# Kernel optimization log

Measured on AMD Instinct MI355X. Metric: run time of the kernel, lower is better.

Reference implementation:

```python
import jax, jax.numpy as jnp
from jax import lax
import numpy as np

EPS = 1e-5

def lc2d(x, w, b, stride):
    # x: [B,H,W]; w: [oh,ow,kh,kw] unshared kernels; b: [oh,ow]
    oh, ow, kh, kw = w.shape
    hi = jnp.arange(oh)[:, None] * stride + jnp.arange(kh)[None, :]  # [oh,kh]
    wi = jnp.arange(ow)[:, None] * stride + jnp.arange(kw)[None, :]  # [ow,kw]
    patches = x[:, hi[:, None, :, None], wi[None, :, None, :]]  # [B,oh,ow,kh,kw]
    return jnp.einsum('bhwkl,hwkl->bhw', patches, w) + b

def ln2d(x, g, b):
    # LayerNorm over last two dims (per-sample)
    m = jnp.mean(x, axis=(-2, -1), keepdims=True)
    v = jnp.var(x, axis=(-2, -1), keepdims=True)
    return (x - m) * lax.rsqrt(v + EPS) * g + b

def maxpool2(x):
    # MaxPool2d(kernel=2, stride=2) on [B,H,W]
    return lax.reduce_window(x, -jnp.inf, lax.max, (1, 2, 2), (1, 2, 2), 'VALID')

def setup_inputs() -> dict:
    key = jax.random.key(0)
    ks = iter(jax.random.split(key, 16))
    d = {'x': jax.random.normal(next(ks), (128, 224, 224), jnp.float32)}
    layer_specs = [(109, 7), (50, 5), (48, 3), (22, 3), (20, 3), (8, 3)]
    for i, (o, k) in enumerate(layer_specs, 1):
        std = float(np.sqrt(2.0 / (k + k)))  # xavier_normal_ on a [k,k] kernel
        d[f'w{i}'] = jax.random.normal(next(ks), (o, o, k, k), jnp.float32) * std
        d[f'b{i}'] = jnp.zeros((o, o), jnp.float32)
        d[f'g{i}'] = jnp.ones((o, o), jnp.float32)
        d[f'be{i}'] = jnp.zeros((o, o), jnp.float32)
    d['fcw'] = jax.random.normal(next(ks), (1000, 64), jnp.float32) * float(np.sqrt(1.0 / 64))
    d['fcb'] = jnp.zeros((1000,), jnp.float32)
    return d

def reference(x, w1, b1, g1, be1, w2, b2, g2, be2, w3, b3, g3, be3,
              w4, b4, g4, be4, w5, b5, g5, be5, w6, b6, g6, be6, fcw, fcb):
    # dropout is inference-mode identity (p=0)
    h = ln2d(jax.nn.relu(lc2d(x, w1, b1, 2)), g1, be1)   # [B,109,109]
    h = maxpool2(h)                                       # [B,54,54]
    h = ln2d(jax.nn.relu(lc2d(h, w2, b2, 1)), g2, be2)   # [B,50,50]
    h = ln2d(jax.nn.relu(lc2d(h, w3, b3, 1)), g3, be3)   # [B,48,48]
    h = maxpool2(h)                                       # [B,24,24]
    h = ln2d(jax.nn.relu(lc2d(h, w4, b4, 1)), g4, be4)   # [B,22,22]
    h = ln2d(jax.nn.relu(lc2d(h, w5, b5, 1)), g5, be5)   # [B,20,20]
    h = maxpool2(h)                                       # [B,10,10]
    h = ln2d(jax.nn.relu(lc2d(h, w6, b6, 1)), g6, be6)   # [B,8,8]
    logits = h.reshape(h.shape[0], -1) @ fcw.T + fcb      # [B,1000]
    return jax.nn.softmax(logits, axis=1)
```

## Files before the change

### kernel.cpp

```cpp
#include <hip/hip_runtime.h>
#include <math.h>

static constexpr float kEps = 1e-5f;

__global__ __launch_bounds__(256)
void xpose(const float* __restrict__ x, float* __restrict__ xt,
           const float* __restrict__ w2, const float* __restrict__ w3,
           const float* __restrict__ w4, const float* __restrict__ w5,
           const float* __restrict__ w6,
           const float* __restrict__ g1, const float* __restrict__ be1,
           float* __restrict__ w2t, float* __restrict__ w3t,
           float* __restrict__ w4t, float* __restrict__ w5t,
           float* __restrict__ w6t,
           float4* __restrict__ g1p, float4* __restrict__ be1p)
{
    const int bid = blockIdx.x, t = threadIdx.x;
    if (bid >= 784) {
        const int tid = (bid - 784) * 256 + t;
        const int nt  = 14 * 256;
        for (int i = tid; i < 25 * 50 * 52; i += nt) {
            const int kk = i / (50 * 52), r = i % (50 * 52);
            const int oh = r / 52, ow = r % 52;
            w2t[i] = (ow < 50) ? w2[(oh * 50 + ow) * 25 + kk] : 0.f;
        }
        for (int i = tid; i < 9 * 2304; i += nt) {
            const int kk = i / 2304, idx = i % 2304;
            w3t[i] = w3[idx * 9 + kk];
        }
        for (int i = tid; i < 9 * 22 * 24; i += nt) {
            const int kk = i / (22 * 24), r = i % (22 * 24);
            const int oh = r / 24, ow = r % 24;
            w4t[i] = (ow < 22) ? w4[(oh * 22 + ow) * 9 + kk] : 0.f;
        }
        for (int i = tid; i < 9 * 400; i += nt) {
            const int kk = i / 400, idx = i % 400;
            w5t[i] = w5[idx * 9 + kk];
        }
        for (int i = tid; i < 9 * 64; i += nt) {
            const int kk = i / 64, idx = i % 64;
            w6t[i] = w6[idx * 9 + kk];
        }
        for (int i = tid; i < 54 * 54; i += nt) {
            const int ph = i / 54, pw = i - ph * 54;
            const int i00 = (2 * ph) * 109 + 2 * pw, i10 = i00 + 109;
            g1p[i]  = make_float4(g1[i00],  g1[i00 + 1],  g1[i10],  g1[i10 + 1]);
            be1p[i] = make_float4(be1[i00], be1[i00 + 1], be1[i10], be1[i10 + 1]);
        }
        return;
    }

    __shared__ float ls[64 * 133];
    const int pos0 = bid * 64;
    for (int i = t; i < 8192; i += 256) {
        const int s = i >> 6, j = i & 63;
        ls[j * 133 + s] = x[(size_t)s * 50176 + pos0 + j];
    }
    __syncthreads();
    for (int i = t; i < 8192; i += 256) {
        const int j = i >> 7, s = i & 127;
        xt[(size_t)(pos0 + j) * 128 + s] = ls[j * 133 + s];
    }
}

__global__ __launch_bounds__(512)
void conv1(const float* __restrict__ xt, const float* __restrict__ w1,
           const float* __restrict__ bias, float* __restrict__ y,
           float* __restrict__ partial)
{
    __shared__ float redS[8][64], redQ[8][64];
    const int oh = blockIdx.x;
    const int grp = blockIdx.y;
    const int t = threadIdx.x;
    const int w = t >> 6, lane = t & 63;
    const int smp = grp * 64 + lane;

    float lsum = 0.f, lsq = 0.f;
    for (int ch = w; ch < 28; ch += 8) {
        const int ow0 = ch * 4;
        float xv[7][13];
        const size_t base = ((size_t)(2 * oh) * 224 + 2 * ow0) * 128 + smp;
        #pragma unroll
        for (int r = 0; r < 7; ++r) {
            #pragma unroll
            for (int c = 0; c < 13; ++c)
                xv[r][c] = xt[base + ((size_t)(r * 224 + c)) * 128];
        }
        #pragma unroll
        for (int o = 0; o < 4; ++o) {
            const int ow = ow0 + o;
            if (ow < 109) {
                const int idx = __builtin_amdgcn_readfirstlane(oh * 109 + ow);
                const float* __restrict__ wr = w1 + (size_t)idx * 49;
                float acc = bias[idx];
                #pragma unroll
                for (int kh = 0; kh < 7; ++kh) {
                    #pragma unroll
                    for (int kw = 0; kw < 7; ++kw)
                        acc = fmaf(xv[kh][2 * o + kw], wr[kh * 7 + kw], acc);
                }
                const float v = fmaxf(acc, 0.f);
                y[((size_t)smp * 109 + oh) * 112 + ow] = v;
                lsum += v; lsq = fmaf(v, v, lsq);
            }
        }
    }
    redS[w][lane] = lsum; redQ[w][lane] = lsq;
    __syncthreads();
    if (w == 0) {
        float s = 0.f, q = 0.f;
        #pragma unroll
        for (int i = 0; i < 8; ++i) { s += redS[i][lane]; q += redQ[i][lane]; }
        *(float2*)(partial + ((size_t)smp * 109 + oh) * 2) = make_float2(s, q);
    }
}

__device__ inline float2 bstats(float ls, float lq, float invN, float (*red)[2], int t)
{
    #pragma unroll
    for (int off = 32; off > 0; off >>= 1) {
        ls += __shfl_down(ls, off, 64);
        lq += __shfl_down(lq, off, 64);
    }
    if ((t & 63) == 0) { red[t >> 6][0] = ls; red[t >> 6][1] = lq; }
    __syncthreads();
    float s = 0.f, q = 0.f;
    #pragma unroll
    for (int w = 0; w < 16; ++w) { s += red[w][0]; q += red[w][1]; }
    const float m = s * invN;
    return make_float2(m, rsqrtf(q * invN - m * m + kEps));
}

__global__ __launch_bounds__(1024)
void tail(const float* __restrict__ y1, const float* __restrict__ partial,
          const float4* __restrict__ g1p, const float4* __restrict__ be1p,
          const float* __restrict__ w2t, const float* __restrict__ b2,
          const float* __restrict__ g2, const float* __restrict__ be2,
          const float* __restrict__ w3t, const float* __restrict__ b3,
          const float* __restrict__ g3, const float* __restrict__ be3,
          const float* __restrict__ w4t, const float* __restrict__ b4,
          const float* __restrict__ g4, const float* __restrict__ be4,
          const float* __restrict__ w5t, const float* __restrict__ b5,
          const float* __restrict__ g5, const float* __restrict__ be5,
          const float* __restrict__ w6t, const float* __restrict__ b6,
          const float* __restrict__ g6, const float* __restrict__ be6,
          const float* __restrict__ fcw, const float* __restrict__ fcb,
          float* __restrict__ out)
{
    __shared__ __align__(16) float xs54[54 * 54 + 8];
    __shared__ __align__(16) float y50[50 * 52];
    __shared__ __align__(16) float y48[48 * 48];
    __shared__ __align__(16) float xs24[24 * 24 + 8];
    __shared__ __align__(16) float y22[22 * 24];
    __shared__ __align__(16) float y20[20 * 20];
    __shared__ __align__(16) float xs10[100];
    __shared__ float y8[64], h[64];
    __shared__ float red[16][2];

    const int b = blockIdx.x, t = threadIdx.x;
    const int lane = t & 63;

    float s, q;
    {
        const float2 p = *(const float2*)(partial + ((size_t)b * 109 + lane) * 2);
        s = p.x; q = p.y;
        if (lane < 45) {
            const float2 p2 = *(const float2*)(partial + ((size_t)b * 109 + 64 + lane) * 2);
            s += p2.x; q += p2.y;
        }
    }
    #pragma unroll
    for (int off = 32; off > 0; off >>= 1) {
        s += __shfl_down(s, off, 64);
        q += __shfl_down(q, off, 64);
    }
    s = __shfl(s, 0, 64); q = __shfl(q, 0, 64);
    const float m1 = s / 11881.f;
    const float r1 = rsqrtf(q / 11881.f - m1 * m1 + kEps);

    const float* yb = y1 + (size_t)b * 109 * 112;
    #pragma unroll
    for (int it = 0; it < 3; ++it) {
        const int idx = t + it * 1024;
        if (idx < 54 * 54) {
            const int ph = idx / 54, pw = idx - ph * 54;
            const int r0 = 2 * ph, c0 = 2 * pw;
            const float2 u0 = *(const float2*)(yb + r0 * 112 + c0);
            const float2 u1 = *(const float2*)(yb + (r0 + 1) * 112 + c0);
            const float4 g = g1p[idx], be = be1p[idx];
            const float v0 = (u0.x - m1) * r1 * g.x + be.x;
            const float v1 = (u0.y - m1) * r1 * g.y + be.y;
            const float v2 = (u1.x - m1) * r1 * g.z + be.z;
            const float v3 = (u1.y - m1) * r1 * g.w + be.w;
            xs54[ph * 54 + pw] = fmaxf(fmaxf(v0, v1), fmaxf(v2, v3));
        }
    }
    __syncthreads();

    float ls = 0.f, lq = 0.f;
    if (t < 650) {
        const int oh = t / 13, qc = t - oh * 13;
        const int ow0 = qc * 4;
        float acc[4];
        #pragma unroll
        for (int o = 0; o < 4; ++o) acc[o] = (ow0 + o < 50) ? b2[oh * 50 + ow0 + o] : 0.f;
        #pragma unroll
        for (int kh = 0; kh < 5; ++kh) {
            const float* xp = xs54 + (oh + kh) * 54 + ow0;
            float a[8];
            #pragma unroll
            for (int i = 0; i < 4; ++i) {
                const float2 v = *(const float2*)(xp + 2 * i);
                a[2 * i] = v.x; a[2 * i + 1] = v.y;
            }
            #pragma unroll
            for (int kw = 0; kw < 5; ++kw) {
                const float4 w4 = *(const float4*)(w2t + ((size_t)(kh * 5 + kw) * 50 + oh) * 52 + ow0);
                acc[0] = fmaf(a[kw    ], w4.x, acc[0]);
                acc[1] = fmaf(a[kw + 1], w4.y, acc[1]);
                acc[2] = fmaf(a[kw + 2], w4.z, acc[2]);
                acc[3] = fmaf(a[kw + 3], w4.w, acc[3]);
            }
        }
        #pragma unroll
        for (int o = 0; o < 4; ++o) {
            const float v = fmaxf(acc[o], 0.f);
            y50[oh * 52 + ow0 + o] = v;
            if (ow0 + o < 50) { ls += v; lq = fmaf(v, v, lq); }
        }
    }
    const float2 s2 = bstats(ls, lq, 1.f / 2500.f, red, t);

    #pragma unroll
    for (int it = 0; it < 3; ++it) {
        const int idx = t + it * 1024;
        if (idx < 2500) {
            const int oh = idx / 50, ow = idx - oh * 50;
            const int p = oh * 52 + ow;
            y50[p] = (y50[p] - s2.x) * s2.y * g2[idx] + be2[idx];
        }
    }
    __syncthreads();

    ls = 0.f; lq = 0.f;
    if (t < 576) {
        const int oh = t / 12, qc = t - oh * 12;
        const int ow0 = qc * 4;
        float acc[4];
        #pragma unroll
        for (int o = 0; o < 4; ++o) acc[o] = b3[oh * 48 + ow0 + o];
        #pragma unroll
        for (int kh = 0; kh < 3; ++kh) {
            const float* xp = y50 + (oh + kh) * 52 + ow0;
            float a[6];
            #pragma unroll
            for (int i = 0; i < 3; ++i) {
                const float2 v = *(const float2*)(xp + 2 * i);
                a[2 * i] = v.x; a[2 * i + 1] = v.y;
            }
            #pragma unroll
            for (int kw = 0; kw < 3; ++kw) {
                const float4 w4 = *(const float4*)(w3t + (size_t)(kh * 3 + kw) * 2304 + oh * 48 + ow0);
                acc[0] = fmaf(a[kw    ], w4.x, acc[0]);
                acc[1] = fmaf(a[kw + 1], w4.y, acc[1]);
                acc[2] = fmaf(a[kw + 2], w4.z, acc[2]);
                acc[3] = fmaf(a[kw + 3], w4.w, acc[3]);
            }
        }
        float4 st;
        #pragma unroll
        for (int o = 0; o < 4; ++o) {
            const float v = fmaxf(acc[o], 0.f);
            (&st.x)[o] = v; ls += v; lq = fmaf(v, v, lq);
        }
        *(float4*)(y48 + oh * 48 + ow0) = st;
    }
    const float2 s3 = bstats(ls, lq, 1.f / 2304.f, red, t);

    if (t < 576) {
        const int ph = t / 24, pw = t - ph * 24;
        const int r0 = 2 * ph, c0 = 2 * pw;
        const float2 u0 = *(const float2*)(y48 + r0 * 48 + c0);
        const float2 u1 = *(const float2*)(y48 + (r0 + 1) * 48 + c0);
        const int i00 = r0 * 48 + c0, i10 = i00 + 48;
        const float v0 = (u0.x - s3.x) * s3.y * g3[i00]     + be3[i00];
        const float v1 = (u0.y - s3.x) * s3.y * g3[i00 + 1] + be3[i00 + 1];
        const float v2 = (u1.x - s3.x) * s3.y * g3[i10]     + be3[i10];
        const float v3 = (u1.y - s3.x) * s3.y * g3[i10 + 1] + be3[i10 + 1];
        xs24[ph * 24 + pw] = fmaxf(fmaxf(v0, v1), fmaxf(v2, v3));
    }
    __syncthreads();

    ls = 0.f; lq = 0.f;
    if (t < 132) {
        const int oh = t / 6, qc = t - oh * 6;
        const int ow0 = qc * 4;
        float acc[4];
        #pragma unroll
        for (int o = 0; o < 4; ++o) acc[o] = (ow0 + o < 22) ? b4[oh * 22 + ow0 + o] : 0.f;
        #pragma unroll
        for (int kh = 0; kh < 3; ++kh) {
            const float* xp = xs24 + (oh + kh) * 24 + ow0;
            float a[6];
            #pragma unroll
            for (int i = 0; i < 3; ++i) {
                const float2 v = *(const float2*)(xp + 2 * i);
                a[2 * i] = v.x; a[2 * i + 1] = v.y;
            }
            #pragma unroll
            for (int kw = 0; kw < 3; ++kw) {
                const float4 w4 = *(const float4*)(w4t + ((size_t)(kh * 3 + kw) * 22 + oh) * 24 + ow0);
                acc[0] = fmaf(a[kw    ], w4.x, acc[0]);
                acc[1] = fmaf(a[kw + 1], w4.y, acc[1]);
                acc[2] = fmaf(a[kw + 2], w4.z, acc[2]);
                acc[3] = fmaf(a[kw + 3], w4.w, acc[3]);
            }
        }
        #pragma unroll
        for (int o = 0; o < 4; ++o) {
            const float v = fmaxf(acc[o], 0.f);
            y22[oh * 24 + ow0 + o] = v;
            if (ow0 + o < 22) { ls += v; lq = fmaf(v, v, lq); }
        }
    }
    const float2 s4 = bstats(ls, lq, 1.f / 484.f, red, t);

    if (t < 484) {
        const int oh = t / 22, ow = t - oh * 22;
        const int p = oh * 24 + ow;
        y22[p] = (y22[p] - s4.x) * s4.y * g4[t] + be4[t];
    }
    __syncthreads();

    ls = 0.f; lq = 0.f;
    if (t < 100) {
        const int oh = t / 5, qc = t - oh * 5;
        const int ow0 = qc * 4;
        float acc[4];
        #pragma unroll
        for (int o = 0; o < 4; ++o) acc[o] = b5[oh * 20 + ow0 + o];
        #pragma unroll
        for (int kh = 0; kh < 3; ++kh) {
            const float* xp = y22 + (oh + kh) * 24 + ow0;
            float a[6];
            #pragma unroll
            for (int i = 0; i < 3; ++i) {
                const float2 v = *(const float2*)(xp + 2 * i);
                a[2 * i] = v.x; a[2 * i + 1] = v.y;
            }
            #pragma unroll
            for (int kw = 0; kw < 3; ++kw) {
                const float4 w4 = *(const float4*)(w5t + (size_t)(kh * 3 + kw) * 400 + oh * 20 + ow0);
                acc[0] = fmaf(a[kw    ], w4.x, acc[0]);
                acc[1] = fmaf(a[kw + 1], w4.y, acc[1]);
                acc[2] = fmaf(a[kw + 2], w4.z, acc[2]);
                acc[3] = fmaf(a[kw + 3], w4.w, acc[3]);
            }
        }
        #pragma unroll
        for (int o = 0; o < 4; ++o) {
            const float v = fmaxf(acc[o], 0.f);
            y20[oh * 20 + ow0 + o] = v;
            ls += v; lq = fmaf(v, v, lq);
        }
    }
    const float2 s5 = bstats(ls, lq, 1.f / 400.f, red, t);

    if (t < 100) {
        const int ph = t / 10, pw = t - ph * 10;
        const int r0 = 2 * ph, c0 = 2 * pw;
        const float2 u0 = *(const float2*)(y20 + r0 * 20 + c0);
        const float2 u1 = *(const float2*)(y20 + (r0 + 1) * 20 + c0);
        const int i00 = r0 * 20 + c0, i10 = i00 + 20;
        const float v0 = (u0.x - s5.x) * s5.y * g5[i00]     + be5[i00];
        const float v1 = (u0.y - s5.x) * s5.y * g5[i00 + 1] + be5[i00 + 1];
        const float v2 = (u1.x - s5.x) * s5.y * g5[i10]     + be5[i10];
        const float v3 = (u1.y - s5.x) * s5.y * g5[i10 + 1] + be5[i10 + 1];
        xs10[ph * 10 + pw] = fmaxf(fmaxf(v0, v1), fmaxf(v2, v3));
    }
    __syncthreads();

    ls = 0.f; lq = 0.f;
    if (t < 16) {
        const int oh = t / 2, qc = t - oh * 2;
        const int ow0 = qc * 4;
        float acc[4];
        #pragma unroll
        for (int o = 0; o < 4; ++o) acc[o] = b6[oh * 8 + ow0 + o];
        #pragma unroll
        for (int kh = 0; kh < 3; ++kh) {
            const float* xp = xs10 + (oh + kh) * 10 + ow0;
            float a[6];
            #pragma unroll
            for (int i = 0; i < 3; ++i) {
                const float2 v = *(const float2*)(xp + 2 * i);
                a[2 * i] = v.x; a[2 * i + 1] = v.y;
            }
            #pragma unroll
            for (int kw = 0; kw < 3; ++kw) {
                const float4 w4 = *(const float4*)(w6t + (size_t)(kh * 3 + kw) * 64 + oh * 8 + ow0);
                acc[0] = fmaf(a[kw    ], w4.x, acc[0]);
                acc[1] = fmaf(a[kw + 1], w4.y, acc[1]);
                acc[2] = fmaf(a[kw + 2], w4.z, acc[2]);
                acc[3] = fmaf(a[kw + 3], w4.w, acc[3]);
            }
        }
        #pragma unroll
        for (int o = 0; o < 4; ++o) {
            const float v = fmaxf(acc[o], 0.f);
            y8[oh * 8 + ow0 + o] = v;
            ls += v; lq = fmaf(v, v, lq);
        }
    }
    const float2 s6 = bstats(ls, lq, 1.f / 64.f, red, t);

    if (t < 64) h[t] = (y8[t] - s6.x) * s6.y * g6[t] + be6[t];
    __syncthreads();

    float lj = -INFINITY;
    if (t < 1000) {
        const float4* wr = (const float4*)(fcw + (size_t)t * 64);
        float acc = fcb[t];
        #pragma unroll
        for (int k = 0; k < 16; ++k) {
            const float4 w4 = wr[k];
            acc = fmaf(h[4 * k], w4.x,
                  fmaf(h[4 * k + 1], w4.y,
                  fmaf(h[4 * k + 2], w4.z,
                  fmaf(h[4 * k + 3], w4.w, acc))));
        }
        lj = acc;
    }
    float mx = lj;
    #pragma unroll
    for (int off = 32; off > 0; off >>= 1) mx = fmaxf(mx, __shfl_down(mx, off, 64));
    if (lane == 0) red[t >> 6][0] = mx;
    __syncthreads();
    float gmax = red[0][0];
    #pragma unroll
    for (int w = 1; w < 16; ++w) gmax = fmaxf(gmax, red[w][0]);

    const float e = (t < 1000) ? __expf(lj - gmax) : 0.f;
    float ssum = e;
    #pragma unroll
    for (int off = 32; off > 0; off >>= 1) ssum += __shfl_down(ssum, off, 64);
    if (lane == 0) red[t >> 6][1] = ssum;
    __syncthreads();
    float tot = 0.f;
    #pragma unroll
    for (int w = 0; w < 16; ++w) tot += red[w][1];
    if (t < 1000) out[(size_t)b * 1000 + t] = e / tot;
}

extern "C" void kernel_launch(void* const* d_in, const int* in_sizes, int n_in,
                              void* d_out, int out_size, void* d_ws, size_t ws_size,
                              hipStream_t stream) {
    const float* x   = (const float*)d_in[0];
    const float* w1  = (const float*)d_in[1];
    const float* b1  = (const float*)d_in[2];
    const float* g1  = (const float*)d_in[3];
    const float* be1 = (const float*)d_in[4];
    const float* w2  = (const float*)d_in[5];
    const float* b2  = (const float*)d_in[6];
    const float* g2  = (const float*)d_in[7];
    const float* be2 = (const float*)d_in[8];
    const float* w3  = (const float*)d_in[9];
    const float* b3  = (const float*)d_in[10];
    const float* g3  = (const float*)d_in[11];
    const float* be3 = (const float*)d_in[12];
    const float* w4  = (const float*)d_in[13];
    const float* b4  = (const float*)d_in[14];
    const float* g4  = (const float*)d_in[15];
    const float* be4 = (const float*)d_in[16];
    const float* w5  = (const float*)d_in[17];
    const float* b5  = (const float*)d_in[18];
    const float* g5  = (const float*)d_in[19];
    const float* be5 = (const float*)d_in[20];
    const float* w6  = (const float*)d_in[21];
    const float* b6  = (const float*)d_in[22];
    const float* g6  = (const float*)d_in[23];
    const float* be6 = (const float*)d_in[24];
    const float* fcw = (const float*)d_in[25];
    const float* fcb = (const float*)d_in[26];

    float* xt   = (float*)d_ws;
    float* y1p  = xt   + 6422528;
    float* w2t  = y1p  + 1562624;
    float* w3t  = w2t  + 65000;
    float* w4t  = w3t  + 20736;
    float* w5t  = w4t  + 4752;
    float* w6t  = w5t  + 3600;
    float* part = w6t  + 576;
    float* g1pp = part + 27904;
    float* be1pp= g1pp + 11664;

    xpose<<<798, 256, 0, stream>>>(x, xt,
                                   w2, w3, w4, w5, w6, g1, be1,
                                   w2t, w3t, w4t, w5t, w6t,
                                   (float4*)g1pp, (float4*)be1pp);

    conv1<<<dim3(109, 2), 512, 0, stream>>>(xt, w1, b1, y1p, part);

    tail<<<128, 1024, 0, stream>>>(y1p, part,
                                   (const float4*)g1pp, (const float4*)be1pp,
                                   w2t, b2, g2, be2,
                                   w3t, b3, g3, be3,
                                   w4t, b4, g4, be4,
                                   w5t, b5, g5, be5,
                                   w6t, b6, g6, be6,
                                   fcw, fcb, (float*)d_out);
}
```

Before: 64.65 us.

## Retile conv1 into 2D output tiles with shared-memory input staging

conv1 now launches a 3D grid of 16x37x2 blocks. Each block covers a 3-row by 7-column output tile for 64 samples, and it stages the overlapping input window into shared memory as float2 pairs before computing. Before, each thread loaded 91 values per 4 outputs straight from global memory, so this cuts redundant global reads and spreads work over more blocks (1184 instead of 218) to use the GPU better. The per-row partial stats become per-tile partials (592 per sample), and the tail kernel now reduces them with a block-wide bstats call. In exchange this adds more partial traffic, uses about 56KB of LDS per block, and leaves some threads idle on edge tiles.

```diff
diff --git a/kernel.cpp b/kernel.cpp
--- a/kernel.cpp
+++ b/kernel.cpp
@@ -62,55 +62,95 @@
     }
 }
 
-__global__ __launch_bounds__(512)
+__global__ __launch_bounds__(384)
 void conv1(const float* __restrict__ xt, const float* __restrict__ w1,
            const float* __restrict__ bias, float* __restrict__ y,
            float* __restrict__ partial)
 {
-    __shared__ float redS[8][64], redQ[8][64];
-    const int oh = blockIdx.x;
-    const int grp = blockIdx.y;
+    constexpr int NPB = 592;
+    __shared__ float2 xin2[11 * 10 * 64];
+    __shared__ float redS[6][64], redQ[6][64];
+
+    const int ct = blockIdx.x;
+    const int rg = blockIdx.y;
+    const int sg = blockIdx.z;
     const int t = threadIdx.x;
-    const int w = t >> 6, lane = t & 63;
-    const int smp = grp * 64 + lane;
+    const int w = t >> 6, s = t & 63;
+    const int smp0 = sg * 64;
+    const int ow0 = ct * 7;
+    const int or0 = rg * 3;
+    const int ih0 = or0 * 2;
+    const int ic0 = ow0 * 2;
+
+    for (int i = t; i < 7040; i += 384) {
+        const int seg = i >> 6, ls = i & 63;
+        const int r = seg / 10, cp = seg - r * 10;
+        const int row = min(ih0 + r, 223);
+        const int c0 = ic0 + 2 * cp;
+        const int ca = min(c0, 223), cb = min(c0 + 1, 223);
+        const float vx = xt[((size_t)row * 224 + ca) * 128 + smp0 + ls];
+        const float vy = xt[((size_t)row * 224 + cb) * 128 + smp0 + ls];
+        xin2[seg * 64 + ls] = make_float2(vx, vy);
+    }
+    __syncthreads();
 
     float lsum = 0.f, lsq = 0.f;
-    for (int ch = w; ch < 28; ch += 8) {
-        const int ow0 = ch * 4;
-        float xv[7][13];
-        const size_t base = ((size_t)(2 * oh) * 224 + 2 * ow0) * 128 + smp;
-        #pragma unroll
-        for (int r = 0; r < 7; ++r) {
-            #pragma unroll
-            for (int c = 0; c < 13; ++c)
-                xv[r][c] = xt[base + ((size_t)(r * 224 + c)) * 128];
-        }
-        #pragma unroll
-        for (int o = 0; o < 4; ++o) {
-            const int ow = ow0 + o;
-            if (ow < 109) {
-                const int idx = __builtin_amdgcn_readfirstlane(oh * 109 + ow);
-                const float* __restrict__ wr = w1 + (size_t)idx * 49;
-                float acc = bias[idx];
+    {
+        const int r = w >> 1, half = w & 1;
+        const int orow = or0 + r;
+        const int oc0 = half ? 3 : 0;
+        const int noc = half ? 4 : 3;
+        const int pr0 = half ? 3 : 0;
+        const int npr = half ? 7 : 6;
+        if (orow < 109) {
+            float acc[4];
+            int idxo[4];
+            #pragma unroll
+            for (int oc = 0; oc < 4; ++oc) {
+                const int ow = ow0 + oc0 + oc;
+                idxo[oc] = __builtin_amdgcn_readfirstlane(orow * 109 + min(ow, 108));
+                acc[oc] = bias[idxo[oc]];
+            }
+            #pragma unroll
+            for (int kh = 0; kh < 7; ++kh) {
+                const int r2 = 2 * r + kh;
+                float xr[14];
                 #pragma unroll
-                for (int kh = 0; kh < 7; ++kh) {
-                    #pragma unroll
-                    for (int kw = 0; kw < 7; ++kw)
-                        acc = fmaf(xv[kh][2 * o + kw], wr[kh * 7 + kw], acc);
+                for (int j = 0; j < 7; ++j) {
+                    if (j < npr) {
+                        const float2 p = xin2[(r2 * 10 + pr0 + j) * 64 + s];
+                        xr[2 * j] = p.x; xr[2 * j + 1] = p.y;
+                    }
                 }
-                const float v = fmaxf(acc, 0.f);
-                y[((size_t)smp * 109 + oh) * 112 + ow] = v;
-                lsum += v; lsq = fmaf(v, v, lsq);
-            }
-        }
-    }
-    redS[w][lane] = lsum; redQ[w][lane] = lsq;
+                #pragma unroll
+                for (int oc = 0; oc < 4; ++oc) {
+                    if (oc < noc) {
+                        const float* __restrict__ wr = w1 + (size_t)idxo[oc] * 49 + kh * 7;
+                        #pragma unroll
+                        for (int kw = 0; kw < 7; ++kw)
+                            acc[oc] = fmaf(xr[2 * oc + kw], wr[kw], acc[oc]);
+                    }
+                }
+            }
+            #pragma unroll
+            for (int oc = 0; oc < 4; ++oc) {
+                const int ow = ow0 + oc0 + oc;
+                if (oc < noc && ow < 109) {
+                    const float v = fmaxf(acc[oc], 0.f);
+                    y[((size_t)(smp0 + s) * 109 + orow) * 112 + ow] = v;
+                    lsum += v; lsq = fmaf(v, v, lsq);
+                }
+            }
+        }
+    }
+    redS[w][s] = lsum; redQ[w][s] = lsq;
     __syncthreads();
     if (w == 0) {
-        float s = 0.f, q = 0.f;
-        #pragma unroll
-        for (int i = 0; i < 8; ++i) { s += redS[i][lane]; q += redQ[i][lane]; }
-        *(float2*)(partial + ((size_t)smp * 109 + oh) * 2) = make_float2(s, q);
+        float ss = 0.f, qq = 0.f;
+        #pragma unroll
+        for (int i = 0; i < 6; ++i) { ss += redS[i][s]; qq += redQ[i][s]; }
+        const int pidx = rg * 16 + ct;
+        *(float2*)(partial + ((size_t)(smp0 + s) * NPB + pidx) * 2) = make_float2(ss, qq);
     }
 }
 
@@ -159,23 +199,13 @@
     const int b = blockIdx.x, t = threadIdx.x;
     const int lane = t & 63;
 
-    float s, q;
-    {
-        const float2 p = *(const float2*)(partial + ((size_t)b * 109 + lane) * 2);
-        s = p.x; q = p.y;
-        if (lane < 45) {
-            const float2 p2 = *(const float2*)(partial + ((size_t)b * 109 + 64 + lane) * 2);
-            s += p2.x; q += p2.y;
-        }
-    }
-    #pragma unroll
-    for (int off = 32; off > 0; off >>= 1) {
-        s += __shfl_down(s, off, 64);
-        q += __shfl_down(q, off, 64);
-    }
-    s = __shfl(s, 0, 64); q = __shfl(q, 0, 64);
-    const float m1 = s / 11881.f;
-    const float r1 = rsqrtf(q / 11881.f - m1 * m1 + kEps);
+    float s0 = 0.f, q0 = 0.f;
+    if (t < 592) {
+        const float2 p = *(const float2*)(partial + ((size_t)b * 592 + t) * 2);
+        s0 = p.x; q0 = p.y;
+    }
+    const float2 st1 = bstats(s0, q0, 1.f / 11881.f, red, t);
+    const float m1 = st1.x, r1 = st1.y;
 
     const float* yb = y1 + (size_t)b * 109 * 112;
     #pragma unroll
@@ -490,7 +520,7 @@
     float* w5t  = w4t  + 4752;
     float* w6t  = w5t  + 3600;
     float* part = w6t  + 576;
-    float* g1pp = part + 27904;
+    float* g1pp = part + 151552;
     float* be1pp= g1pp + 11664;
 
     xpose<<<798, 256, 0, stream>>>(x, xt,
@@ -498,7 +528,7 @@
                                    w2t, w3t, w4t, w5t, w6t,
                                    (float4*)g1pp, (float4*)be1pp);
 
-    conv1<<<dim3(109, 2), 512, 0, stream>>>(xt, w1, b1, y1p, part);
+    conv1<<<dim3(16, 37, 2), 384, 0, stream>>>(xt, w1, b1, y1p, part);
 
     tail<<<128, 1024, 0, stream>>>(y1p, part,
                                    (const float4*)g1pp, (const float4*)be1pp,
```

Result: slower. 82.76 us (+28.0%).

## Register-block conv1 over 4x4 output tiles with rolling input rows and coalesced stores

Applied to the files above, without the earlier changes.

conv1 now has each thread compute a 4x4 block of output positions. Input rows stream through a double-buffered 13-element register window, so each loaded row feeds up to four output rows instead of being reloaded per output row. Outputs are staged in shared memory and written as float4 rows, replacing scattered scalar stores. The grid is reshaped to 7x28x2 blocks of 256 threads, and the per-sample partial statistics grow to 196 entries, which tail now reduces with the block-wide bstats helper. The cost is a smaller grid with more register pressure per thread, plus some redundant clamped work at the edges.

```diff
diff --git a/kernel.cpp b/kernel.cpp
--- a/kernel.cpp
+++ b/kernel.cpp
@@ -62,55 +62,98 @@
     }
 }
 
-__global__ __launch_bounds__(512)
+__global__ __launch_bounds__(256)
 void conv1(const float* __restrict__ xt, const float* __restrict__ w1,
            const float* __restrict__ bias, float* __restrict__ y,
            float* __restrict__ partial)
 {
-    __shared__ float redS[8][64], redQ[8][64];
-    const int oh = blockIdx.x;
-    const int grp = blockIdx.y;
-    const int t = threadIdx.x;
-    const int w = t >> 6, lane = t & 63;
+    __shared__ float ytile[64 * 67];
+    __shared__ float redS[4][64], redQ[4][64];
+
+    const int cg = blockIdx.x;
+    const int rg = blockIdx.y;
+    const int grp = blockIdx.z;
+    const int t = threadIdx.x, w = t >> 6, lane = t & 63;
     const int smp = grp * 64 + lane;
-
-    float lsum = 0.f, lsq = 0.f;
-    for (int ch = w; ch < 28; ch += 8) {
-        const int ow0 = ch * 4;
-        float xv[7][13];
-        const size_t base = ((size_t)(2 * oh) * 224 + 2 * ow0) * 128 + smp;
-        #pragma unroll
-        for (int r = 0; r < 7; ++r) {
+    const int or0 = rg * 4;
+    const int ow0 = cg * 16 + w * 4;
+    const int ih0 = or0 * 2, ic0 = ow0 * 2;
+
+    float acc[4][4];
+    int idxo[4][4];
+    #pragma unroll
+    for (int a = 0; a < 4; ++a) {
+        #pragma unroll
+        for (int oc = 0; oc < 4; ++oc) {
+            const int orow = min(or0 + a, 108), ow = min(ow0 + oc, 108);
+            idxo[a][oc] = __builtin_amdgcn_readfirstlane(orow * 109 + ow);
+            acc[a][oc] = bias[idxo[a][oc]];
+        }
+    }
+
+    float cur[13], nxt[13];
+    {
+        const int rr = min(ih0, 223);
+        #pragma unroll
+        for (int c = 0; c < 13; ++c)
+            cur[c] = xt[((size_t)rr * 224 + min(ic0 + c, 223)) * 128 + smp];
+    }
+    #pragma unroll 1
+    for (int r = 0; r < 13; ++r) {
+        if (r < 12) {
+            const int rr = min(ih0 + r + 1, 223);
             #pragma unroll
             for (int c = 0; c < 13; ++c)
-                xv[r][c] = xt[base + ((size_t)(r * 224 + c)) * 128];
-        }
-        #pragma unroll
-        for (int o = 0; o < 4; ++o) {
-            const int ow = ow0 + o;
-            if (ow < 109) {
-                const int idx = __builtin_amdgcn_readfirstlane(oh * 109 + ow);
-                const float* __restrict__ wr = w1 + (size_t)idx * 49;
-                float acc = bias[idx];
+                nxt[c] = xt[((size_t)rr * 224 + min(ic0 + c, 223)) * 128 + smp];
+        }
+        #pragma unroll
+        for (int a = 0; a < 4; ++a) {
+            const int kh = r - 2 * a;
+            if (kh >= 0 && kh < 7) {
                 #pragma unroll
-                for (int kh = 0; kh < 7; ++kh) {
+                for (int oc = 0; oc < 4; ++oc) {
+                    const float* __restrict__ wr = w1 + (size_t)idxo[a][oc] * 49 + kh * 7;
                     #pragma unroll
                     for (int kw = 0; kw < 7; ++kw)
-                        acc = fmaf(xv[kh][2 * o + kw], wr[kh * 7 + kw], acc);
+                        acc[a][oc] = fmaf(cur[2 * oc + kw], wr[kw], acc[a][oc]);
                 }
-                const float v = fmaxf(acc, 0.f);
-                y[((size_t)smp * 109 + oh) * 112 + ow] = v;
+            }
+        }
+        #pragma unroll
+        for (int c = 0; c < 13; ++c) cur[c] = nxt[c];
+    }
+
+    float lsum = 0.f, lsq = 0.f;
+    #pragma unroll
+    for (int a = 0; a < 4; ++a) {
+        #pragma unroll
+        for (int oc = 0; oc < 4; ++oc) {
+            const int orow = or0 + a, ow = ow0 + oc;
+            float v = fmaxf(acc[a][oc], 0.f);
+            if (orow < 109 && ow < 109) {
                 lsum += v; lsq = fmaf(v, v, lsq);
-            }
+            } else v = 0.f;
+            ytile[lane * 67 + a * 16 + (w * 4 + oc)] = v;
         }
     }
     redS[w][lane] = lsum; redQ[w][lane] = lsq;
     __syncthreads();
+
+    for (int i = t; i < 1024; i += 256) {
+        const int pair = i >> 2, k = i & 3;
+        const int sl = pair >> 2, a = pair & 3;
+        const int orow = or0 + a;
+        if (orow < 109) {
+            const int c = a * 16 + k * 4;
+            const float4 vv = make_float4(ytile[sl * 67 + c],     ytile[sl * 67 + c + 1],
+                                          ytile[sl * 67 + c + 2], ytile[sl * 67 + c + 3]);
+            *(float4*)(y + ((size_t)(grp * 64 + sl) * 109 + orow) * 112 + cg * 16 + k * 4) = vv;
+        }
+    }
     if (w == 0) {
-        float s = 0.f, q = 0.f;
-        #pragma unroll
-        for (int i = 0; i < 8; ++i) { s += redS[i][lane]; q += redQ[i][lane]; }
-        *(float2*)(partial + ((size_t)smp * 109 + oh) * 2) = make_float2(s, q);
+        const float s = redS[0][lane] + redS[1][lane] + redS[2][lane] + redS[3][lane];
+        const float q = redQ[0][lane] + redQ[1][lane] + redQ[2][lane] + redQ[3][lane];
+        *(float2*)(partial + ((size_t)smp * 196 + rg * 7 + cg) * 2) = make_float2(s, q);
     }
 }
 
@@ -159,23 +202,13 @@
     const int b = blockIdx.x, t = threadIdx.x;
     const int lane = t & 63;
 
-    float s, q;
-    {
-        const float2 p = *(const float2*)(partial + ((size_t)b * 109 + lane) * 2);
-        s = p.x; q = p.y;
-        if (lane < 45) {
-            const float2 p2 = *(const float2*)(partial + ((size_t)b * 109 + 64 + lane) * 2);
-            s += p2.x; q += p2.y;
-        }
-    }
-    #pragma unroll
-    for (int off = 32; off > 0; off >>= 1) {
-        s += __shfl_down(s, off, 64);
-        q += __shfl_down(q, off, 64);
-    }
-    s = __shfl(s, 0, 64); q = __shfl(q, 0, 64);
-    const float m1 = s / 11881.f;
-    const float r1 = rsqrtf(q / 11881.f - m1 * m1 + kEps);
+    float s0 = 0.f, q0 = 0.f;
+    if (t < 196) {
+        const float2 p = *(const float2*)(partial + ((size_t)b * 196 + t) * 2);
+        s0 = p.x; q0 = p.y;
+    }
+    const float2 st1 = bstats(s0, q0, 1.f / 11881.f, red, t);
+    const float m1 = st1.x, r1 = st1.y;
 
     const float* yb = y1 + (size_t)b * 109 * 112;
     #pragma unroll
@@ -490,7 +523,7 @@
     float* w5t  = w4t  + 4752;
     float* w6t  = w5t  + 3600;
     float* part = w6t  + 576;
-    float* g1pp = part + 27904;
+    float* g1pp = part + 50176;
     float* be1pp= g1pp + 11664;
 
     xpose<<<798, 256, 0, stream>>>(x, xt,
@@ -498,7 +531,7 @@
                                    w2t, w3t, w4t, w5t, w6t,
                                    (float4*)g1pp, (float4*)be1pp);
 
-    conv1<<<dim3(109, 2), 512, 0, stream>>>(xt, w1, b1, y1p, part);
+    conv1<<<dim3(7, 28, 2), 256, 0, stream>>>(xt, w1, b1, y1p, part);
 
     tail<<<128, 1024, 0, stream>>>(y1p, part,
                                    (const float4*)g1pp, (const float4*)be1pp,
```

Result: slower. 66.57 us (+3.0%).
